# Performance work log

Measured on AMD Instinct MI355X. Metric: run time of the kernel, lower is better.

Reference implementation:

```python
import jax, jax.numpy as jnp
import numpy as np

N = 100000
E = 1600000
D_IN = 64
D_HID = 64


def gcn_layer(x, W, b, src, dst, n):
    # PyG GCNConv: h = D^{-1/2} (A + I) D^{-1/2} (x W) + b
    h = x @ W                                   # [N, d_out]
    deg = jnp.zeros((n,), x.dtype).at[dst].add(1.0) + 1.0  # in-degree + self loop
    dinv = jax.lax.rsqrt(deg)                   # deg >= 1 so safe
    norm = dinv[src] * dinv[dst]                # [E]
    msg = h[src] * norm[:, None]                # gather + scale, [E, d_out]
    out = jax.ops.segment_sum(msg, dst, num_segments=n)  # scatter-add
    out = out + h * (dinv * dinv)[:, None]      # self-loop term
    return out + b


def setup_inputs() -> dict:
    key = jax.random.key(0)
    ks = jax.random.split(key, 8)
    x = jax.random.normal(ks[0], (N, D_IN), dtype=jnp.float32)
    edge_index = jax.random.randint(ks[1], (2, E), 0, N, dtype=jnp.int64)
    s = 1.0 / np.sqrt(D_IN)
    W1 = jax.random.uniform(ks[2], (D_IN, D_HID), jnp.float32, -s, s)
    b1 = jnp.zeros((D_HID,), jnp.float32)
    s2 = 1.0 / np.sqrt(D_HID)
    W2 = jax.random.uniform(ks[3], (D_HID, D_HID), jnp.float32, -s2, s2)
    b2 = jnp.zeros((D_HID,), jnp.float32)
    W3 = jax.random.uniform(ks[4], (D_HID, 1), jnp.float32, -s2, s2)
    b3 = jnp.zeros((1,), jnp.float32)
    return {"x": x, "edge_index": edge_index, "W1": W1, "b1": b1,
            "W2": W2, "b2": b2, "W3": W3, "b3": b3}


def reference(x, edge_index, W1, b1, W2, b2, W3, b3):
    src, dst = edge_index[0], edge_index[1]
    n = x.shape[0]
    # dropout(p=0.1) is identity in eval mode
    h = jax.nn.relu(gcn_layer(x, W1, b1, src, dst, n))
    h = jax.nn.relu(gcn_layer(h, W2, b2, src, dst, n))
    out = gcn_layer(h, W3, b3, src, dst, n)     # [N, 1]
    return out
```

## Files before the change

kernel.cpp:

```cpp
#include <hip/hip_runtime.h>


#define THREADS 256
#define NPB_SHIFT 9
#define NPB 512
#define BCAP 9216
#define STAGE_CAP 9216

__global__ __launch_bounds__(THREADS) void k_bscat2(
    const int* __restrict__ src, const int* __restrict__ dst,
    int* __restrict__ bucketCur, int* __restrict__ eb, int E) {
  __shared__ int hist[4][256];
  __shared__ int hcur[256];
  int t = threadIdx.x;
  for (int j = t; j < 1024; j += THREADS) ((int*)hist)[j] = 0;
  __syncthreads();
  int blockStart = blockIdx.x * 4096;
  int sub = t & 3;
#pragma unroll
  for (int c = 0; c < 4; c++) {
    int e0 = blockStart + c * 1024 + t * 4;
    if (e0 + 3 < E) {
      int4 d = *(const int4*)(dst + e0);
      atomicAdd(&hist[sub][d.x >> NPB_SHIFT], 1);
      atomicAdd(&hist[sub][d.y >> NPB_SHIFT], 1);
      atomicAdd(&hist[sub][d.z >> NPB_SHIFT], 1);
      atomicAdd(&hist[sub][d.w >> NPB_SHIFT], 1);
    } else {
      int lim = min(e0 + 4, E);
      for (int e = e0; e < lim; e++) atomicAdd(&hist[sub][dst[e] >> NPB_SHIFT], 1);
    }
  }
  __syncthreads();
  int cnt = hist[0][t] + hist[1][t] + hist[2][t] + hist[3][t];
  int rb = 0;
  if (cnt) rb = atomicAdd(&bucketCur[t], cnt);
  __syncthreads();
  hcur[t] = rb;
  __syncthreads();
#pragma unroll
  for (int c = 0; c < 4; c++) {
    int e0 = blockStart + c * 1024 + t * 4;
    if (e0 + 3 < E) {
      int4 s = *(const int4*)(src + e0);
      int4 d = *(const int4*)(dst + e0);
      int b, q;
      b = d.x >> NPB_SHIFT; q = atomicAdd(&hcur[b], 1);
      eb[b * BCAP + q] = ((d.x & (NPB - 1)) << 17) | s.x;
      b = d.y >> NPB_SHIFT; q = atomicAdd(&hcur[b], 1);
      eb[b * BCAP + q] = ((d.y & (NPB - 1)) << 17) | s.y;
      b = d.z >> NPB_SHIFT; q = atomicAdd(&hcur[b], 1);
      eb[b * BCAP + q] = ((d.z & (NPB - 1)) << 17) | s.z;
      b = d.w >> NPB_SHIFT; q = atomicAdd(&hcur[b], 1);
      eb[b * BCAP + q] = ((d.w & (NPB - 1)) << 17) | s.w;
    } else {
      int lim = min(e0 + 4, E);
      for (int e = e0; e < lim; e++) {
        int dd = dst[e];
        int b = dd >> NPB_SHIFT;
        int q = atomicAdd(&hcur[b], 1);
        eb[b * BCAP + q] = ((dd & (NPB - 1)) << 17) | src[e];
      }
    }
  }
}

__global__ __launch_bounds__(THREADS) void k_bscan2(
    const int* __restrict__ bucketCur, int* __restrict__ bucketOff,
    int* __restrict__ rowptr, int n, int E, int nbuck) {
  __shared__ int sh[THREADS];
  int t = threadIdx.x;
  int v = (t < nbuck) ? bucketCur[t] : 0;
  sh[t] = v;
  __syncthreads();
  for (int off = 1; off < THREADS; off <<= 1) {
    int u = (t >= off) ? sh[t - off] : 0;
    __syncthreads();
    sh[t] += u;
    __syncthreads();
  }
  bucketOff[t] = sh[t] - v;
  if (t == 0) {
    bucketOff[nbuck] = E;
    rowptr[n] = E;
  }
}

__global__ __launch_bounds__(THREADS) void k_bcsr3(
    const int* __restrict__ eb, const int* __restrict__ bucketCur,
    const int* __restrict__ bucketOff, int* __restrict__ rowptr,
    float* __restrict__ dinv, int* __restrict__ es, int n) {
  __shared__ int lcnt4[4][NPB];
  __shared__ int lcnt[NPB];
  __shared__ int sA[NPB];
  __shared__ int sB[NPB];
  __shared__ int lcur[NPB];
  __shared__ int stage[STAGE_CAP];
  int b = blockIdx.x;
  int t = threadIdx.x;
  int cntB = bucketCur[b];
  int baseIn = b * BCAP;
  int baseOut = bucketOff[b];
  int node0 = b << NPB_SHIFT;
  int nn = min(NPB, n - node0);
  int sub = t & 3;

  for (int j = t; j < 4 * NPB; j += THREADS) ((int*)lcnt4)[j] = 0;
  __syncthreads();
  for (int p = t; p < cntB; p += THREADS) {
    int v = eb[baseIn + p];
    atomicAdd(&lcnt4[sub][v >> 17], 1);
  }
  __syncthreads();
#pragma unroll
  for (int k = 0; k < 2; k++) {
    int j = t + k * 256;
    lcnt[j] = lcnt4[0][j] + lcnt4[1][j] + lcnt4[2][j] + lcnt4[3][j];
  }
  __syncthreads();
  sA[t] = lcnt[t]; sA[t + 256] = lcnt[t + 256];
  __syncthreads();
  int* bin = sA; int* bout = sB;
  for (int off = 1; off < NPB; off <<= 1) {
    int j0 = t, j1 = t + 256;
    int a0 = bin[j0] + ((j0 >= off) ? bin[j0 - off] : 0);
    int a1 = bin[j1] + ((j1 >= off) ? bin[j1 - off] : 0);
    bout[j0] = a0; bout[j1] = a1;
    __syncthreads();
    int* tmp = bin; bin = bout; bout = tmp;
  }
#pragma unroll
  for (int k = 0; k < 2; k++) {
    int j = t + k * 256;
    if (j < nn) {
      int c = lcnt[j];
      int ex = bin[j] - c;
      rowptr[node0 + j] = baseOut + ex;
      dinv[node0 + j] = rsqrtf((float)c + 1.f);
      lcur[j] = ex;
    }
  }
  __syncthreads();
  for (int p = t; p < cntB; p += THREADS) {
    int v = eb[baseIn + p];
    int q = atomicAdd(&lcur[v >> 17], 1);
    if (q < STAGE_CAP) stage[q] = v & 0x1FFFF;
  }
  __syncthreads();
  int lim = min(cntB, STAGE_CAP);
  for (int q = t; q < lim; q += THREADS) es[baseOut + q] = stage[q];
}

__global__ __launch_bounds__(THREADS) void k_gemmT(
    const float* __restrict__ A, const float* __restrict__ W,
    const float* __restrict__ dinv, float* __restrict__ C, int n) {
  __shared__ float At[16 * 64];
  int t = threadIdx.x;
  int lane = t & 63;
  int wid = t >> 6;

  float w[64];
#pragma unroll
  for (int k = 0; k < 64; k++) w[k] = W[k * 64 + lane];

  int ntiles = (n + 15) >> 4;
  for (int tile = blockIdx.x; tile < ntiles; tile += gridDim.x) {
    int row0 = tile << 4;
    {
      int r = row0 + (t >> 4);
      float4 v = make_float4(0.f, 0.f, 0.f, 0.f);
      if (r < n) v = ((const float4*)(A + (size_t)row0 * 64))[t];
      ((float4*)At)[t] = v;
    }
    __syncthreads();

#pragma unroll
    for (int j = 0; j < 4; j++) {
      int lr = wid * 4 + j;
      int r = row0 + lr;
      float acc0 = 0.f, acc1 = 0.f, acc2 = 0.f, acc3 = 0.f;
#pragma unroll
      for (int q = 0; q < 4; q++) {
        float4 a0 = *(const float4*)&At[lr * 64 + q * 16 + 0];
        float4 a1 = *(const float4*)&At[lr * 64 + q * 16 + 4];
        float4 a2 = *(const float4*)&At[lr * 64 + q * 16 + 8];
        float4 a3 = *(const float4*)&At[lr * 64 + q * 16 + 12];
        int k0 = q * 16;
        acc0 = fmaf(a0.x, w[k0 + 0],  acc0);
        acc1 = fmaf(a0.y, w[k0 + 1],  acc1);
        acc2 = fmaf(a0.z, w[k0 + 2],  acc2);
        acc3 = fmaf(a0.w, w[k0 + 3],  acc3);
        acc0 = fmaf(a1.x, w[k0 + 4],  acc0);
        acc1 = fmaf(a1.y, w[k0 + 5],  acc1);
        acc2 = fmaf(a1.z, w[k0 + 6],  acc2);
        acc3 = fmaf(a1.w, w[k0 + 7],  acc3);
        acc0 = fmaf(a2.x, w[k0 + 8],  acc0);
        acc1 = fmaf(a2.y, w[k0 + 9],  acc1);
        acc2 = fmaf(a2.z, w[k0 + 10], acc2);
        acc3 = fmaf(a2.w, w[k0 + 11], acc3);
        acc0 = fmaf(a3.x, w[k0 + 12], acc0);
        acc1 = fmaf(a3.y, w[k0 + 13], acc1);
        acc2 = fmaf(a3.z, w[k0 + 14], acc2);
        acc3 = fmaf(a3.w, w[k0 + 15], acc3);
      }
      if (r < n)
        C[(size_t)r * 64 + lane] = ((acc0 + acc1) + (acc2 + acc3)) * dinv[r];
    }
    __syncthreads();
  }
}

template <int RELU>
__global__ __launch_bounds__(THREADS) void k_agg64(
    const float* __restrict__ hs, const float* __restrict__ dinv,
    const int* __restrict__ rowptr, const int* __restrict__ es,
    const float* __restrict__ b, float* __restrict__ out, int n) {
  int lane = threadIdx.x & 63;
  int g = lane >> 4;
  int c = lane & 15;
  int gw = (int)((blockIdx.x * THREADS + threadIdx.x) >> 6);
  int nw = (gridDim.x * THREADS) >> 6;
  const float4* h4 = (const float4*)hs;
  float4 bb = ((const float4*)b)[c];

  for (int i = gw; i < n; i += nw) {
    int p1 = rowptr[i + 1];
    int p = rowptr[i] + g;
    float4 acc  = make_float4(0.f, 0.f, 0.f, 0.f);
    float4 acc1 = make_float4(0.f, 0.f, 0.f, 0.f);
    float4 acc2 = make_float4(0.f, 0.f, 0.f, 0.f);
    float4 acc3 = make_float4(0.f, 0.f, 0.f, 0.f);
    for (; p + 12 < p1; p += 16) {
      int s0 = es[p];
      int s1 = es[p + 4];
      int s2 = es[p + 8];
      int s3 = es[p + 12];
      float4 v0 = h4[(size_t)s0 * 16 + c];
      float4 v1 = h4[(size_t)s1 * 16 + c];
      float4 v2 = h4[(size_t)s2 * 16 + c];
      float4 v3 = h4[(size_t)s3 * 16 + c];
      acc.x  += v0.x; acc.y  += v0.y; acc.z  += v0.z; acc.w  += v0.w;
      acc1.x += v1.x; acc1.y += v1.y; acc1.z += v1.z; acc1.w += v1.w;
      acc2.x += v2.x; acc2.y += v2.y; acc2.z += v2.z; acc2.w += v2.w;
      acc3.x += v3.x; acc3.y += v3.y; acc3.z += v3.z; acc3.w += v3.w;
    }
    for (; p + 4 < p1; p += 8) {
      int s0 = es[p];
      int s1 = es[p + 4];
      float4 v0 = h4[(size_t)s0 * 16 + c];
      float4 v1 = h4[(size_t)s1 * 16 + c];
      acc.x  += v0.x; acc.y  += v0.y; acc.z  += v0.z; acc.w  += v0.w;
      acc1.x += v1.x; acc1.y += v1.y; acc1.z += v1.z; acc1.w += v1.w;
    }
    if (p < p1) {
      int s0 = es[p];
      float4 v0 = h4[(size_t)s0 * 16 + c];
      acc.x += v0.x; acc.y += v0.y; acc.z += v0.z; acc.w += v0.w;
    }
    acc.x += acc1.x + acc2.x + acc3.x;
    acc.y += acc1.y + acc2.y + acc3.y;
    acc.z += acc1.z + acc2.z + acc3.z;
    acc.w += acc1.w + acc2.w + acc3.w;
#pragma unroll
    for (int m = 16; m <= 32; m <<= 1) {
      acc.x += __shfl_xor(acc.x, m, 64);
      acc.y += __shfl_xor(acc.y, m, 64);
      acc.z += __shfl_xor(acc.z, m, 64);
      acc.w += __shfl_xor(acc.w, m, 64);
    }
    if (g == 0) {
      float di = dinv[i];
      float4 self = h4[(size_t)i * 16 + c];
      float4 r;
      r.x = di * (acc.x + self.x) + bb.x;
      r.y = di * (acc.y + self.y) + bb.y;
      r.z = di * (acc.z + self.z) + bb.z;
      r.w = di * (acc.w + self.w) + bb.w;
      if (RELU) {
        r.x = fmaxf(r.x, 0.f); r.y = fmaxf(r.y, 0.f);
        r.z = fmaxf(r.z, 0.f); r.w = fmaxf(r.w, 0.f);
      }
      ((float4*)out)[(size_t)i * 16 + c] = r;
    }
  }
}

__global__ __launch_bounds__(THREADS) void k_gemv(
    const float* __restrict__ a2, const float* __restrict__ W3,
    const float* __restrict__ dinv, float* __restrict__ g3, int n) {
  int t = blockIdx.x * blockDim.x + threadIdx.x;
  int i = t >> 4, p = t & 15;
  if (i >= n) return;
  float4 v = ((const float4*)a2)[t];
  float4 w = ((const float4*)W3)[p];
  float sum = v.x * w.x + v.y * w.y + v.z * w.z + v.w * w.w;
  sum += __shfl_down(sum, 8, 16);
  sum += __shfl_down(sum, 4, 16);
  sum += __shfl_down(sum, 2, 16);
  sum += __shfl_down(sum, 1, 16);
  if (p == 0) g3[i] = sum * dinv[i];
}

__global__ __launch_bounds__(THREADS) void k_agg1(
    const float* __restrict__ g3, const float* __restrict__ dinv,
    const int* __restrict__ rowptr, const int* __restrict__ es,
    const float* __restrict__ b3, float* __restrict__ out, int n) {
  int i = blockIdx.x * blockDim.x + threadIdx.x;
  if (i >= n) return;
  int p = rowptr[i], p1 = rowptr[i + 1];
  float acc = 0.f, accb = 0.f;
  for (; p + 1 < p1; p += 2) {
    acc  += g3[es[p]];
    accb += g3[es[p + 1]];
  }
  if (p < p1) acc += g3[es[p]];
  out[i] = dinv[i] * (acc + accb + g3[i]) + b3[0];
}

extern "C" void kernel_launch(void* const* d_in, const int* in_sizes, int n_in,
                              void* d_out, int out_size, void* d_ws, size_t ws_size,
                              hipStream_t stream) {
  const float* x  = (const float*)d_in[0];
  const int*   ei = (const int*)d_in[1];
  const float* W1 = (const float*)d_in[2];
  const float* b1 = (const float*)d_in[3];
  const float* W2 = (const float*)d_in[4];
  const float* b2 = (const float*)d_in[5];
  const float* W3 = (const float*)d_in[6];
  const float* b3 = (const float*)d_in[7];
  float* out = (float*)d_out;

  const int n = in_sizes[0] / 64;
  const int E = in_sizes[1] / 2;
  const int* src = ei;
  const int* dst = ei + E;
  const int nbuck = (n + NPB - 1) >> NPB_SHIFT;
  const int nA = (E + 4095) / 4096;

  char* w = (char*)d_ws;
  auto alloc = [&](size_t bytes) -> void* {
    void* p = (void*)w;
    w += (bytes + 255) & ~(size_t)255;
    return p;
  };
  int*   bucketCur = (int*)alloc(256 * 4);
  int*   bucketOff = (int*)alloc(257 * 4);
  int*   rowptr    = (int*)alloc(((size_t)n + 1) * 4);
  int*   eb        = (int*)alloc((size_t)256 * BCAP * 4);
  int*   es        = (int*)alloc((size_t)E * 4);
  float* dinv      = (float*)alloc((size_t)n * 4);
  float* g3        = (float*)alloc((size_t)n * 4);
  float* bufA      = (float*)alloc((size_t)n * 64 * 4);
  float* bufB      = (float*)alloc((size_t)n * 64 * 4);

  const int gN    = (n + THREADS - 1) / THREADS;
  const int gN16  = ((n * 16) + THREADS - 1) / THREADS;
  const int gGemm = 1024;
  const int gAgg  = 2048;

  hipMemsetAsync(bucketCur, 0, 256 * 4, stream);
  k_bscat2<<<nA, THREADS, 0, stream>>>(src, dst, bucketCur, eb, E);
  k_bscan2<<<1, THREADS, 0, stream>>>(bucketCur, bucketOff, rowptr, n, E, nbuck);
  k_bcsr3<<<nbuck, THREADS, 0, stream>>>(eb, bucketCur, bucketOff, rowptr, dinv, es, n);

  k_gemmT<<<gGemm, THREADS, 0, stream>>>(x, W1, dinv, bufA, n);
  k_agg64<1><<<gAgg, THREADS, 0, stream>>>(bufA, dinv, rowptr, es, b1, bufB, n);
  k_gemmT<<<gGemm, THREADS, 0, stream>>>(bufB, W2, dinv, bufA, n);
  k_agg64<1><<<gAgg, THREADS, 0, stream>>>(bufA, dinv, rowptr, es, b2, bufB, n);
  k_gemv<<<gN16, THREADS, 0, stream>>>(bufB, W3, dinv, g3, n);
  k_agg1<<<gN, THREADS, 0, stream>>>(g3, dinv, rowptr, es, b3, out, n);
}
```

Before: 236.4 us.

## Fuse next-layer GEMM and GEMV into the aggregation kernel epilogues

The layer-1 aggregation kernel now applies bias and ReLU, stages each row in shared memory, and multiplies it by W2 held in registers. It writes the prescaled input for layer 2 directly, removing the separate GEMM pass and one full round trip of the N×64 activations through memory. The layer-2 aggregation likewise fuses the W3 dot product via a wave reduction, replacing the separate GEMV kernel. The cost is 64 extra registers per thread for W2, which may lower occupancy in a gather-bound kernel, plus extra compute and a shared-memory hop per node.

```diff
diff --git a/kernel.cpp b/kernel.cpp
--- a/kernel.cpp
+++ b/kernel.cpp
@@ -210,18 +210,30 @@
   }
 }
 
-template <int RELU>
-__global__ __launch_bounds__(THREADS) void k_agg64(
+template <int MODE>
+__global__ __launch_bounds__(THREADS) void k_agg64f(
     const float* __restrict__ hs, const float* __restrict__ dinv,
     const int* __restrict__ rowptr, const int* __restrict__ es,
-    const float* __restrict__ b, float* __restrict__ out, int n) {
-  int lane = threadIdx.x & 63;
+    const float* __restrict__ b, const float* __restrict__ Wn,
+    float* __restrict__ out, int n) {
+  __shared__ float rowbuf[4][64];
+  int t = threadIdx.x;
+  int lane = t & 63;
   int g = lane >> 4;
   int c = lane & 15;
-  int gw = (int)((blockIdx.x * THREADS + threadIdx.x) >> 6);
+  int wid = t >> 6;
+  int gw = (int)((blockIdx.x * THREADS + t) >> 6);
   int nw = (gridDim.x * THREADS) >> 6;
   const float4* h4 = (const float4*)hs;
   float4 bb = ((const float4*)b)[c];
+
+  float w[MODE == 1 ? 64 : 1];
+  if (MODE == 1) {
+#pragma unroll
+    for (int k = 0; k < 64; k++) w[k] = Wn[k * 64 + lane];
+  } else {
+    w[0] = Wn[lane];
+  }
 
   for (int i = gw; i < n; i += nw) {
     int p1 = rowptr[i + 1];
@@ -268,37 +280,51 @@
       acc.z += __shfl_xor(acc.z, m, 64);
       acc.w += __shfl_xor(acc.w, m, 64);
     }
+    float di = dinv[i];
     if (g == 0) {
-      float di = dinv[i];
       float4 self = h4[(size_t)i * 16 + c];
-      float4 r;
-      r.x = di * (acc.x + self.x) + bb.x;
-      r.y = di * (acc.y + self.y) + bb.y;
-      r.z = di * (acc.z + self.z) + bb.z;
-      r.w = di * (acc.w + self.w) + bb.w;
-      if (RELU) {
-        r.x = fmaxf(r.x, 0.f); r.y = fmaxf(r.y, 0.f);
-        r.z = fmaxf(r.z, 0.f); r.w = fmaxf(r.w, 0.f);
+      float4 a;
+      a.x = fmaxf(di * (acc.x + self.x) + bb.x, 0.f);
+      a.y = fmaxf(di * (acc.y + self.y) + bb.y, 0.f);
+      a.z = fmaxf(di * (acc.z + self.z) + bb.z, 0.f);
+      a.w = fmaxf(di * (acc.w + self.w) + bb.w, 0.f);
+      *(float4*)&rowbuf[wid][c * 4] = a;
+    }
+    if (MODE == 1) {
+      const float* rb = rowbuf[wid];
+      float o0 = 0.f, o1 = 0.f, o2 = 0.f, o3 = 0.f;
+#pragma unroll
+      for (int q = 0; q < 4; q++) {
+        float4 a0 = *(const float4*)&rb[q * 16 + 0];
+        float4 a1 = *(const float4*)&rb[q * 16 + 4];
+        float4 a2 = *(const float4*)&rb[q * 16 + 8];
+        float4 a3 = *(const float4*)&rb[q * 16 + 12];
+        int k0 = q * 16;
+        o0 = fmaf(a0.x, w[k0 + 0],  o0);
+        o1 = fmaf(a0.y, w[k0 + 1],  o1);
+        o2 = fmaf(a0.z, w[k0 + 2],  o2);
+        o3 = fmaf(a0.w, w[k0 + 3],  o3);
+        o0 = fmaf(a1.x, w[k0 + 4],  o0);
+        o1 = fmaf(a1.y, w[k0 + 5],  o1);
+        o2 = fmaf(a1.z, w[k0 + 6],  o2);
+        o3 = fmaf(a1.w, w[k0 + 7],  o3);
+        o0 = fmaf(a2.x, w[k0 + 8],  o0);
+        o1 = fmaf(a2.y, w[k0 + 9],  o1);
+        o2 = fmaf(a2.z, w[k0 + 10], o2);
+        o3 = fmaf(a2.w, w[k0 + 11], o3);
+        o0 = fmaf(a3.x, w[k0 + 12], o0);
+        o1 = fmaf(a3.y, w[k0 + 13], o1);
+        o2 = fmaf(a3.z, w[k0 + 14], o2);
+        o3 = fmaf(a3.w, w[k0 + 15], o3);
       }
-      ((float4*)out)[(size_t)i * 16 + c] = r;
-    }
-  }
-}
-
-__global__ __launch_bounds__(THREADS) void k_gemv(
-    const float* __restrict__ a2, const float* __restrict__ W3,
-    const float* __restrict__ dinv, float* __restrict__ g3, int n) {
-  int t = blockIdx.x * blockDim.x + threadIdx.x;
-  int i = t >> 4, p = t & 15;
-  if (i >= n) return;
-  float4 v = ((const float4*)a2)[t];
-  float4 w = ((const float4*)W3)[p];
-  float sum = v.x * w.x + v.y * w.y + v.z * w.z + v.w * w.w;
-  sum += __shfl_down(sum, 8, 16);
-  sum += __shfl_down(sum, 4, 16);
-  sum += __shfl_down(sum, 2, 16);
-  sum += __shfl_down(sum, 1, 16);
-  if (p == 0) g3[i] = sum * dinv[i];
+      out[(size_t)i * 64 + lane] = ((o0 + o1) + (o2 + o3)) * di;
+    } else {
+      float v = rowbuf[wid][lane] * w[0];
+#pragma unroll
+      for (int m = 1; m < 64; m <<= 1) v += __shfl_xor(v, m, 64);
+      if (lane == 0) out[i] = v * di;
+    }
+  }
 }
 
 __global__ __launch_bounds__(THREADS) void k_agg1(
@@ -354,7 +380,6 @@
   float* bufB      = (float*)alloc((size_t)n * 64 * 4);
 
   const int gN    = (n + THREADS - 1) / THREADS;
-  const int gN16  = ((n * 16) + THREADS - 1) / THREADS;
   const int gGemm = 1024;
   const int gAgg  = 2048;
 
@@ -364,9 +389,7 @@
   k_bcsr3<<<nbuck, THREADS, 0, stream>>>(eb, bucketCur, bucketOff, rowptr, dinv, es, n);
 
   k_gemmT<<<gGemm, THREADS, 0, stream>>>(x, W1, dinv, bufA, n);
-  k_agg64<1><<<gAgg, THREADS, 0, stream>>>(bufA, dinv, rowptr, es, b1, bufB, n);
-  k_gemmT<<<gGemm, THREADS, 0, stream>>>(bufB, W2, dinv, bufA, n);
-  k_agg64<1><<<gAgg, THREADS, 0, stream>>>(bufA, dinv, rowptr, es, b2, bufB, n);
-  k_gemv<<<gN16, THREADS, 0, stream>>>(bufB, W3, dinv, g3, n);
+  k_agg64f<1><<<gAgg, THREADS, 0, stream>>>(bufA, dinv, rowptr, es, b1, W2, bufB, n);
+  k_agg64f<2><<<gAgg, THREADS, 0, stream>>>(bufB, dinv, rowptr, es, b2, W3, g3, n);
   k_agg1<<<gN, THREADS, 0, stream>>>(g3, dinv, rowptr, es, b3, out, n);
 }
```

After: 224.0 us. 1.06x faster.
